# Optimization experiments

Hardware: AMD Instinct MI355X
Metric: run time of the kernel (lower is better)

## Reference

```python
import jax, jax.numpy as jnp
import numpy as np

NEG = jnp.float32(-1e30)  # safe stand-in for -inf in log-space

def setup_inputs() -> dict:
    key = jax.random.key(0)
    k1, k2, k3, k4 = jax.random.split(key, 4)
    N, C, T, S = 64, 64, 4000, 100
    logits = jax.random.normal(k1, (N, C, T), dtype=jnp.float32)
    targets = jax.random.randint(k2, (N, S), 1, C)          # labels, no blank
    target_lengths = jax.random.randint(k3, (N,), 1, S + 1)  # >= 1
    input_lengths = jax.random.randint(k4, (N,), 2000, T + 1)
    return {"logits": logits, "targets": targets,
            "target_lengths": target_lengths, "input_lengths": input_lengths}

def _lse2(a, b):
    m = jnp.maximum(a, b)
    return m + jnp.log(jnp.exp(a - m) + jnp.exp(b - m))

def _lse3(a, b, c):
    m = jnp.maximum(jnp.maximum(a, b), c)
    return m + jnp.log(jnp.exp(a - m) + jnp.exp(b - m) + jnp.exp(c - m))

def reference(logits, targets, target_lengths, input_lengths):
    # logits: (N, C, T); blank = 0; reduction = 'mean' (per-sample / target_len, then mean)
    N, C, T = logits.shape
    S = targets.shape[1]
    L = 2 * S + 1
    lp = jax.nn.log_softmax(logits, axis=1)      # (N, C, T)
    lp = jnp.transpose(lp, (2, 0, 1))            # (T, N, C)

    # extended label sequence: blank, t1, blank, t2, ..., blank  -> (N, L)
    ext = jnp.zeros((N, L), dtype=targets.dtype).at[:, 1::2].set(targets)
    # skip transition s-2 -> s allowed iff ext[s] != blank and ext[s] != ext[s-2]
    prev2 = jnp.pad(ext[:, :-2], ((0, 0), (2, 0)), constant_values=0)
    skip_ok = (ext != 0) & (ext != prev2)        # (N, L)

    # per-time log-probs of extended labels: (T, N, L)
    lp_ext = jnp.take_along_axis(lp, jnp.broadcast_to(ext[None], (T, N, L)), axis=2)

    # alpha init at t=0
    alpha = jnp.full((N, L), NEG, dtype=lp.dtype)
    alpha = alpha.at[:, 0].set(lp_ext[0, :, 0])
    alpha = alpha.at[:, 1].set(lp_ext[0, :, 1])

    neg1 = jnp.full((N, 1), NEG, dtype=lp.dtype)
    neg2 = jnp.full((N, 2), NEG, dtype=lp.dtype)

    def step(a, inp):
        lpt, t = inp                              # lpt: (N, L)
        a1 = a
        a2 = jnp.concatenate([neg1, a[:, :-1]], axis=1)
        a3 = jnp.concatenate([neg2, a[:, :-2]], axis=1)
        a3 = jnp.where(skip_ok, a3, NEG)
        new = _lse3(a1, a2, a3) + lpt
        active = (t < input_lengths)[:, None]     # freeze past input length
        return jnp.where(active, new, a), None

    alpha, _ = jax.lax.scan(step, alpha, (lp_ext[1:], jnp.arange(1, T)))

    i1 = (2 * target_lengths)[:, None]            # last blank
    i2 = jnp.maximum(i1 - 1, 0)                   # last label
    v1 = jnp.take_along_axis(alpha, i1, axis=1)[:, 0]
    v2 = jnp.take_along_axis(alpha, i2, axis=1)[:, 0]
    loss_n = -_lse2(v1, v2)                       # (N,)
    return jnp.mean(loss_n / target_lengths.astype(loss_n.dtype))
```

## Files before the change

kernel.cpp:

```cpp
#include <hip/hip_runtime.h>
#include <cstdint>
#include <cstddef>

#define NEGV (-1e30f)
#define IL2f 1.44269504088896340736f
#define LN2f 0.693147180559945309417f

__device__ __forceinline__ float exp2_hw(float x) { return __builtin_amdgcn_exp2f(x); }
__device__ __forceinline__ float log2_hw(float x) { return __builtin_amdgcn_logf(x); }

constexpr int Nn = 64, Cc = 64, Tt = 4000, Ss = 100;

__device__ __forceinline__ float wave_shr1(float x) {
    return __int_as_float(__builtin_amdgcn_update_dpp(0, __float_as_int(x), 0x138, 0xF, 0xF, true));
}
__device__ __forceinline__ float wave_shl1(float x) {
    return __int_as_float(__builtin_amdgcn_update_dpp(0, __float_as_int(x), 0x130, 0xF, 0xF, true));
}
__device__ __forceinline__ int wave_shr1_i(int x) {
    return __builtin_amdgcn_update_dpp(0, x, 0x138, 0xF, 0xF, true);
}
__device__ __forceinline__ int wave_shl1_i(int x) {
    return __builtin_amdgcn_update_dpp(0, x, 0x130, 0xF, 0xF, true);
}

typedef float f4 __attribute__((ext_vector_type(4)));
typedef float f2 __attribute__((ext_vector_type(2)));
#define LD4(p) (*(const f4*)(p))

__device__ __forceinline__ void gload16(const float* g, float* l) {
    __builtin_amdgcn_global_load_lds(
        (const __attribute__((address_space(1))) void*)g,
        (__attribute__((address_space(3))) void*)l, 16, 0, 0);
}

__global__ __launch_bounds__(256) void ctc_softmax_kernel(
    const float* __restrict__ logits, float* __restrict__ d2, float* __restrict__ P)
{
    const int t4 = (blockIdx.x * 256 + threadIdx.x) * 4;
    const int n = blockIdx.y;
    if (t4 >= Tt) return;
    const float* __restrict__ p = logits + (size_t)n * Cc * Tt + t4;
    f4 m, s;
    {
        f4 v = LD4(p);
        #pragma unroll
        for (int i = 0; i < 4; ++i) { m[i] = v[i] * IL2f; s[i] = 1.f; }
    }
    #pragma unroll 4
    for (int c = 1; c < Cc; ++c) {
        f4 v = LD4(p + (size_t)c * Tt);
        #pragma unroll
        for (int i = 0; i < 4; ++i) {
            float vi = v[i] * IL2f;
            float nm = fmaxf(m[i], vi);
            s[i] = s[i] * exp2_hw(m[i] - nm) + exp2_hw(vi - nm);
            m[i] = nm;
        }
    }
    f4 d;
    #pragma unroll
    for (int i = 0; i < 4; ++i) d[i] = m[i] + log2_hw(s[i]);
    *(f4*)(d2 + (size_t)n * Tt + t4) = d;
    if (P) {
        float* __restrict__ dst = P + (size_t)n * Cc * Tt + t4;
        #pragma unroll 4
        for (int c = 0; c < Cc; ++c) {
            f4 v = LD4(p + (size_t)c * Tt);
            f4 o;
            #pragma unroll
            for (int i = 0; i < 4; ++i) o[i] = exp2_hw(fmaf(v[i], IL2f, -d[i]));
            *(f4*)(dst + (size_t)c * Tt) = o;
        }
    }
}

template<bool PRE>
__global__ __launch_bounds__(64) void ctc_fb_kernel(
    const float* __restrict__ PR, const int* __restrict__ targets,
    const int* __restrict__ tlen, const int* __restrict__ ilen,
    const float* __restrict__ d2, float* __restrict__ wsA, float* __restrict__ wsB)
{
    constexpr int NA = PRE ? 3 : 4;
    constexpr int NLD = NA * 4;
    __shared__ float lds[3][NA][4][64][4];

    const int bid = blockIdx.x;
    const int n = bid >> 1;
    const bool bwd = bid & 1;
    const int lane = threadIdx.x;
    const int tl = tlen[n];
    const int Tn = ilen[n];
    const int L = 2 * tl + 1;
    const int mid = Tn >> 1;
    const int s0 = 4 * lane;

    const int j1 = min(2 * lane, Ss - 1);
    const int j3 = min(2 * lane + 1, Ss - 1);
    const int base = n * Ss;
    const int tg1 = targets[base + j1];
    const int tg3 = targets[base + j3];
    const int tg1m = targets[base + max(2 * lane - 1, 0)];
    const int tg3p = targets[base + min(2 * lane + 2, Ss - 1)];

    const float sk1f = ((s0 + 1 >= 3) && (tg1 != tg1m)) ? 1.f : 0.f;
    const float sk3f = (tg3 != tg1) ? 1.f : 0.f;
    const float sk1b = ((s0 + 3 < L) && (tg3 != tg1)) ? 1.f : 0.f;
    const float sk3b = ((s0 + 5 < L) && (tg3p != tg3)) ? 1.f : 0.f;

    const float* __restrict__ rB = PR + (size_t)(n * Cc) * Tt;
    const float* __restrict__ r1 = PR + (size_t)(n * Cc + tg1) * Tt;
    const float* __restrict__ r3 = PR + (size_t)(n * Cc + tg3) * Tt;
    const float* __restrict__ rD = d2 + (size_t)n * Tt;

    float a0, a1, a2, a3;
    int E = 0;

    if (!bwd) {
        float pB0, p10;
        if constexpr (PRE) { pB0 = rB[0]; p10 = r1[0]; }
        else {
            const float dv = rD[0];
            pB0 = exp2_hw(fmaf(rB[0], IL2f, -dv));
            p10 = exp2_hw(fmaf(r1[0], IL2f, -dv));
        }
        a0 = (lane == 0) ? pB0 : 0.f;
        a1 = (lane == 0) ? p10 : 0.f;
        a2 = 0.f; a3 = 0.f;
    } else {
        const int te = Tn - 1;
        float pBe, p1e, p3e;
        if constexpr (PRE) { pBe = rB[te]; p1e = r1[te]; p3e = r3[te]; }
        else {
            const float dv = rD[te];
            pBe = exp2_hw(fmaf(rB[te], IL2f, -dv));
            p1e = exp2_hw(fmaf(r1[te], IL2f, -dv));
            p3e = exp2_hw(fmaf(r3[te], IL2f, -dv));
        }
        const int sl = 2 * tl;
        a0 = (s0 == sl) ? pBe : 0.f;
        a1 = (s0 + 1 == sl - 1) ? p1e : 0.f;
        a2 = (s0 + 2 == sl) ? pBe : 0.f;
        a3 = (s0 + 3 == sl - 1) ? p3e : 0.f;
    }

    #define ISSUE(gg, sl) {                                                         \
        const int bo_ = (gg) * 16;                                                  \
        _Pragma("unroll")                                                           \
        for (int j = 0; j < 4; ++j) {                                               \
            gload16(rB + bo_ + 4 * j, &lds[sl][0][j][0][0]);                        \
            gload16(r1 + bo_ + 4 * j, &lds[sl][1][j][0][0]);                        \
            gload16(r3 + bo_ + 4 * j, &lds[sl][2][j][0][0]);                        \
            if constexpr (!PRE) gload16(rD + bo_ + 4 * j, &lds[sl][NA - 1][j][0][0]); \
        }                                                                           \
    }
    #define WAITG() asm volatile("s_waitcnt vmcnt(%0)" :: "n"(2 * NLD) : "memory")
    #define LOADREGS(slc)                                                           \
        f4 vB[4], vU[4], vW[4], vD[4];                                              \
        _Pragma("unroll")                                                           \
        for (int j = 0; j < 4; ++j) {                                               \
            vB[j] = LD4(&lds[slc][0][j][lane][0]);                                  \
            vU[j] = LD4(&lds[slc][1][j][lane][0]);                                  \
            vW[j] = LD4(&lds[slc][2][j][lane][0]);                                  \
            if constexpr (!PRE) vD[j] = LD4(&lds[slc][NA - 1][j][lane][0]);         \
        }                                                                           \
        (void)vD;

    #define RENORM_S(nb) {                                                          \
        const float mx = fmaxf(fmaxf(a0, a1), fmaxf(a2, a3));                       \
        const int me = (int)(__float_as_uint(mx) >> 23);                            \
        const float s2 = __int_as_float((unsigned)(254 - me) << 23);                \
        a0 *= s2; a1 *= s2; a2 *= s2; a3 *= s2;                                     \
        E = (mx > 0.f) ? (E + me - 127) : (nb);                                     \
    }

    if (!bwd) {
        const int tB = mid;
        const int gHi = tB >> 4;

        #define BODY_F_G(gg) {                                                      \
            _Pragma("unroll")                                                       \
            for (int w = 0; w < 2; ++w) {                                           \
                const int Eu = wave_shr1_i(E);                                      \
                const int eb = min(max(127 + (Eu - E), 0), 230);                    \
                const float sc = __int_as_float((unsigned)eb << 23);                \
                const float sk1fs = sk1f * sc;                                      \
                _Pragma("unroll")                                                   \
                for (int kk = 0; kk < 8; ++kk) {                                    \
                    const int k = w * 8 + kk;                                       \
                    const int t = (gg) * 16 + k;                                    \
                    if (t >= 1 && t <= tB) {                                        \
                        float pB, p1, p3;                                           \
                        if constexpr (PRE) {                                        \
                            pB = vB[k >> 2][k & 3]; p1 = vU[k >> 2][k & 3];         \
                            p3 = vW[k >> 2][k & 3];                                 \
                        } else {                                                    \
                            const float dv = vD[k >> 2][k & 3];                     \
                            pB = exp2_hw(fmaf(vB[k >> 2][k & 3], IL2f, -dv));       \
                            p1 = exp2_hw(fmaf(vU[k >> 2][k & 3], IL2f, -dv));       \
                            p3 = exp2_hw(fmaf(vW[k >> 2][k & 3], IL2f, -dv));       \
                        }                                                           \
                        const float u3 = wave_shr1(a3);                             \
                        const float n3 = fmaf(a1, sk3f, a3 + a2) * p3;              \
                        const float n2 = (a2 + a1) * pB;                            \
                        const float n1 = fmaf(u3, sk1fs, a1 + a0) * p1;             \
                        const float n0 = fmaf(u3, sc, a0) * pB;                     \
                        a0 = n0; a1 = n1; a2 = n2; a3 = n3;                         \
                    }                                                               \
                }                                                                   \
                RENORM_S(Eu);                                                       \
            }                                                                       \
        }

        #define BODY_F_F() {                                                        \
            f2 Q0 = {a0, a2}, Q1 = {a1, a3};                                        \
            _Pragma("unroll")                                                       \
            for (int w = 0; w < 2; ++w) {                                           \
                const int Eu = wave_shr1_i(E);                                      \
                const int eb = min(max(127 + (Eu - E), 0), 230);                    \
                const float sc = __int_as_float((unsigned)eb << 23);                \
                const f2 Ksk = {sk3f, sk1f * sc};                                   \
                const f2 K1s = {1.0f, sc};                                          \
                _Pragma("unroll")                                                   \
                for (int kk = 0; kk < 8; ++kk) {                                    \
                    const int k = w * 8 + kk;                                       \
                    const float pB = vB[k >> 2][k & 3];                             \
                    const f2 P31 = {vW[k >> 2][k & 3], vU[k >> 2][k & 3]};          \
                    const f2 PBB = {pB, pB};                                        \
                    const float u3 = wave_shr1(Q1.y);                               \
                    const f2 M = {Q1.x, u3};                                        \
                    const f2 Q0s = __builtin_shufflevector(Q0, Q0, 1, 0);           \
                    const f2 S = __builtin_shufflevector(Q1, Q1, 1, 0) + Q0s;       \
                    const f2 F = __builtin_elementwise_fma(M, Ksk, S);              \
                    const f2 G = __builtin_elementwise_fma(M, K1s, Q0s);            \
                    const f2 N31 = F * P31;                                         \
                    const f2 N20 = G * PBB;                                         \
                    Q1 = __builtin_shufflevector(N31, N31, 1, 0);                   \
                    Q0 = __builtin_shufflevector(N20, N20, 1, 0);                   \
                }                                                                   \
                const f2 mxv = __builtin_elementwise_max(Q0, Q1);                   \
                const float mx = fmaxf(mxv.x, mxv.y);                               \
                const int me = (int)(__float_as_uint(mx) >> 23);                    \
                const float s2 = __int_as_float((unsigned)(254 - me) << 23);        \
                const f2 S2 = {s2, s2};                                             \
                Q0 *= S2; Q1 *= S2;                                                 \
                E = (mx > 0.f) ? (E + me - 127) : Eu;                               \
            }                                                                       \
            a0 = Q0.x; a2 = Q0.y; a1 = Q1.x; a3 = Q1.y;                             \
        }

        ISSUE(0, 0);
        ISSUE(min(1, gHi), 1);
        int sli = 2, slc = 0;
        for (int g = 0; g <= gHi; ++g) {
            ISSUE(min(g + 2, gHi), sli);
            sli = (sli == 2) ? 0 : sli + 1;
            WAITG();
            LOADREGS(slc);
            slc = (slc == 2) ? 0 : slc + 1;
            if (PRE && g >= 1 && g * 16 + 15 <= tB) { BODY_F_F(); }
            else                                    { BODY_F_G(g); }
        }
        #undef BODY_F_G
        #undef BODY_F_F
    } else {
        const int tB = Tn - 2, tA = mid + 1;
        const int gHi = tB >> 4, gLo = tA >> 4;

        #define BODY_B_G(gg) {                                                      \
            _Pragma("unroll")                                                       \
            for (int w = 1; w >= 0; --w) {                                          \
                const int Ed = wave_shl1_i(E);                                      \
                const int eb = min(max(127 + (Ed - E), 0), 230);                    \
                const float sc = __int_as_float((unsigned)eb << 23);                \
                const float sk3bs = sk3b * sc;                                      \
                _Pragma("unroll")                                                   \
                for (int kk = 7; kk >= 0; --kk) {                                   \
                    const int k = w * 8 + kk;                                       \
                    const int t = (gg) * 16 + k;                                    \
                    if (t >= tA && t <= tB) {                                       \
                        float pB, p1, p3;                                           \
                        if constexpr (PRE) {                                        \
                            pB = vB[k >> 2][k & 3]; p1 = vU[k >> 2][k & 3];         \
                            p3 = vW[k >> 2][k & 3];                                 \
                        } else {                                                    \
                            const float dv = vD[k >> 2][k & 3];                     \
                            pB = exp2_hw(fmaf(vB[k >> 2][k & 3], IL2f, -dv));       \
                            p1 = exp2_hw(fmaf(vU[k >> 2][k & 3], IL2f, -dv));       \
                            p3 = exp2_hw(fmaf(vW[k >> 2][k & 3], IL2f, -dv));       \
                        }                                                           \
                        const float d0 = wave_shl1(a0);                             \
                        const float d1 = wave_shl1(a1);                             \
                        const float n0 = (a0 + a1) * pB;                            \
                        const float n1 = fmaf(a3, sk1b, a1 + a2) * p1;              \
                        const float n2 = (a2 + a3) * pB;                            \
                        const float n3 = fmaf(d1, sk3bs, fmaf(d0, sc, a3)) * p3;    \
                        a0 = n0; a1 = n1; a2 = n2; a3 = n3;                         \
                    }                                                               \
                }                                                                   \
                RENORM_S(Ed);                                                       \
            }                                                                       \
        }

        #define BODY_B_F() {                                                        \
            f2 Q0 = {a0, a2}, Q1 = {a1, a3};                                        \
            _Pragma("unroll")                                                       \
            for (int w = 1; w >= 0; --w) {                                          \
                const int Ed = wave_shl1_i(E);                                      \
                const int eb = min(max(127 + (Ed - E), 0), 230);                    \
                const float sc = __int_as_float((unsigned)eb << 23);                \
                const f2 K1s = {1.0f, sc};                                          \
                const f2 Ksk = {sk1b, sk3b * sc};                                   \
                _Pragma("unroll")                                                   \
                for (int kk = 7; kk >= 0; --kk) {                                   \
                    const int k = w * 8 + kk;                                       \
                    const float pB = vB[k >> 2][k & 3];                             \
                    const f2 P13 = {vU[k >> 2][k & 3], vW[k >> 2][k & 3]};          \
                    const f2 PBB = {pB, pB};                                        \
                    const float d0 = wave_shl1(Q0.x);                               \
                    const float d1 = wave_shl1(Q1.x);                               \
                    const f2 S = Q0 + Q1;                                           \
                    const f2 A2 = __builtin_elementwise_fma((f2){Q0.y, d0}, K1s, Q1); \
                    const f2 B2 = __builtin_elementwise_fma((f2){Q1.y, d1}, Ksk, A2); \
                    Q1 = B2 * P13;                                                  \
                    Q0 = S * PBB;                                                   \
                }                                                                   \
                const f2 mxv = __builtin_elementwise_max(Q0, Q1);                   \
                const float mx = fmaxf(mxv.x, mxv.y);                               \
                const int me = (int)(__float_as_uint(mx) >> 23);                    \
                const float s2 = __int_as_float((unsigned)(254 - me) << 23);        \
                const f2 S2 = {s2, s2};                                             \
                Q0 *= S2; Q1 *= S2;                                                 \
                E = (mx > 0.f) ? (E + me - 127) : Ed;                               \
            }                                                                       \
            a0 = Q0.x; a2 = Q0.y; a1 = Q1.x; a3 = Q1.y;                             \
        }

        ISSUE(gHi, 0);
        ISSUE(max(gHi - 1, 0), 1);
        int sli = 2, slc = 0;
        for (int g = gHi; g >= gLo; --g) {
            ISSUE(max(g - 2, 0), sli);
            sli = (sli == 2) ? 0 : sli + 1;
            WAITG();
            LOADREGS(slc);
            slc = (slc == 2) ? 0 : slc + 1;
            if (PRE && g * 16 >= tA && g * 16 + 15 <= tB) { BODY_B_F(); }
            else                                          { BODY_B_G(g); }
        }
        #undef BODY_B_G
        #undef BODY_B_F
    }
    #undef ISSUE
    #undef WAITG
    #undef LOADREGS
    #undef RENORM_S

    float* dst = (bwd ? wsB : wsA) + n * 256;
    const float Ef = (float)E;
    f4 o;
    o[0] = (s0     < L && a0 > 0.f) ? log2_hw(a0) + Ef : NEGV;
    o[1] = (s0 + 1 < L && a1 > 0.f) ? log2_hw(a1) + Ef : NEGV;
    o[2] = (s0 + 2 < L && a2 > 0.f) ? log2_hw(a2) + Ef : NEGV;
    o[3] = (s0 + 3 < L && a3 > 0.f) ? log2_hw(a3) + Ef : NEGV;
    *(f4*)(dst + s0) = o;
}

__global__ __launch_bounds__(64) void ctc_combine_kernel(
    const float* __restrict__ wsA, const float* __restrict__ wsB,
    const int* __restrict__ targets, const int* __restrict__ tlen,
    float* __restrict__ out)
{
    const int n = blockIdx.x;
    const int lane = threadIdx.x;
    const int tl = tlen[n];
    const int L = 2 * tl + 1;
    float vals[4];
    float vmax = NEGV;
    #pragma unroll
    for (int k = 0; k < 4; ++k) {
        const int s = lane + (k << 6);
        float v = NEGV;
        if (s < L) {
            const float al = wsA[n * 256 + s];
            const float b0 = wsB[n * 256 + s];
            const float b1 = (s + 1 < L) ? wsB[n * 256 + s + 1] : NEGV;
            const bool skip = (s & 1) && (s + 2 < L) &&
                (targets[n * Ss + (s >> 1) + 1] != targets[n * Ss + (s >> 1)]);
            const float b2 = skip ? wsB[n * 256 + s + 2] : NEGV;
            const float m3 = fmaxf(fmaxf(b0, b1), b2);
            const float B = m3 + log2_hw(exp2_hw(b0 - m3) + exp2_hw(b1 - m3) + exp2_hw(b2 - m3));
            v = al + B;
        }
        vals[k] = v;
        vmax = fmaxf(vmax, v);
    }
    #pragma unroll
    for (int o = 32; o; o >>= 1) vmax = fmaxf(vmax, __shfl_xor(vmax, o));
    float ssum = 0.f;
    #pragma unroll
    for (int k = 0; k < 4; ++k) ssum += exp2_hw(vals[k] - vmax);
    #pragma unroll
    for (int o = 32; o; o >>= 1) ssum += __shfl_xor(ssum, o);
    if (lane == 0) {
        const float total2 = vmax + log2_hw(ssum);
        const float loss = -LN2f * total2;
        atomicAdd(out, loss / ((float)tl * (float)Nn));
    }
}

extern "C" void kernel_launch(void* const* d_in, const int* in_sizes, int n_in,
                              void* d_out, int out_size, void* d_ws, size_t ws_size,
                              hipStream_t stream) {
    const float* logits = (const float*)d_in[0];
    const int* targets  = (const int*)d_in[1];
    const int* tlen     = (const int*)d_in[2];
    const int* ilen     = (const int*)d_in[3];
    float* out = (float*)d_out;

    float* wsA = (float*)d_ws;
    float* wsB = wsA + Nn * 256;
    float* d2  = wsB + Nn * 256;
    float* P   = d2 + (size_t)Nn * Tt;
    const size_t need = ((size_t)Nn * 256 * 2 + (size_t)Nn * Tt
                         + (size_t)Nn * Cc * Tt) * sizeof(float);
    const bool pre = (ws_size >= need);

    hipMemsetAsync(d_out, 0, sizeof(float), stream);
    ctc_softmax_kernel<<<dim3(4, Nn), 256, 0, stream>>>(logits, d2, pre ? P : nullptr);
    if (pre) {
        ctc_fb_kernel<true><<<Nn * 2, 64, 0, stream>>>(P, targets, tlen, ilen, d2, wsA, wsB);
    } else {
        ctc_fb_kernel<false><<<Nn * 2, 64, 0, stream>>>(logits, targets, tlen, ilen, d2, wsA, wsB);
    }
    ctc_combine_kernel<<<Nn, 64, 0, stream>>>(wsA, wsB, targets, tlen, out);
}
```

Baseline: 120.3 us.

## Split probability precompute into parallel kernel and double-buffer 32-step chunks

The softmax kernel is split in two: one kernel computes per-time log-denominators, and a new kernel, launched over an extra grid dimension of channel groups, writes the normalized probabilities. This gives the probability pass more parallelism than the single 256-block launch. The forward-backward kernel's async LDS prefetch changes from a triple-buffered 16-timestep pipeline to a double-buffered 32-timestep one, so it issues fewer waits and loop iterations. In exchange it adds a kernel launch, a re-read of the logits, more registers for the larger LOADREGS arrays, and a shallower prefetch depth.

```diff
diff --git a/kernel.cpp b/kernel.cpp
--- a/kernel.cpp
+++ b/kernel.cpp
@@ -34,8 +34,8 @@
         (__attribute__((address_space(3))) void*)l, 16, 0, 0);
 }
 
-__global__ __launch_bounds__(256) void ctc_softmax_kernel(
-    const float* __restrict__ logits, float* __restrict__ d2, float* __restrict__ P)
+__global__ __launch_bounds__(256) void ctc_denom_kernel(
+    const float* __restrict__ logits, float* __restrict__ d2)
 {
     const int t4 = (blockIdx.x * 256 + threadIdx.x) * 4;
     const int n = blockIdx.y;
@@ -58,20 +58,29 @@
             m[i] = nm;
         }
     }
-    f4 d;
-    #pragma unroll
-    for (int i = 0; i < 4; ++i) d[i] = m[i] + log2_hw(s[i]);
-    *(f4*)(d2 + (size_t)n * Tt + t4) = d;
-    if (P) {
-        float* __restrict__ dst = P + (size_t)n * Cc * Tt + t4;
-        #pragma unroll 4
-        for (int c = 0; c < Cc; ++c) {
-            f4 v = LD4(p + (size_t)c * Tt);
-            f4 o;
-            #pragma unroll
-            for (int i = 0; i < 4; ++i) o[i] = exp2_hw(fmaf(v[i], IL2f, -d[i]));
-            *(f4*)(dst + (size_t)c * Tt) = o;
-        }
+    f4 o;
+    #pragma unroll
+    for (int i = 0; i < 4; ++i) o[i] = m[i] + log2_hw(s[i]);
+    *(f4*)(d2 + (size_t)n * Tt + t4) = o;
+}
+
+__global__ __launch_bounds__(256) void ctc_prob_kernel(
+    const float* __restrict__ logits, const float* __restrict__ d2, float* __restrict__ P)
+{
+    const int t4 = (blockIdx.x * 256 + threadIdx.x) * 4;
+    const int n = blockIdx.y;
+    const int c0 = blockIdx.z * 8;
+    if (t4 >= Tt) return;
+    const f4 d = LD4(d2 + (size_t)n * Tt + t4);
+    const float* __restrict__ src = logits + ((size_t)n * Cc + c0) * Tt + t4;
+    float* __restrict__ dst = P + ((size_t)n * Cc + c0) * Tt + t4;
+    #pragma unroll
+    for (int c = 0; c < 8; ++c) {
+        f4 v = LD4(src + (size_t)c * Tt);
+        f4 o;
+        #pragma unroll
+        for (int i = 0; i < 4; ++i) o[i] = exp2_hw(fmaf(v[i], IL2f, -d[i]));
+        *(f4*)(dst + (size_t)c * Tt) = o;
     }
 }
 
@@ -82,8 +91,8 @@
     const float* __restrict__ d2, float* __restrict__ wsA, float* __restrict__ wsB)
 {
     constexpr int NA = PRE ? 3 : 4;
-    constexpr int NLD = NA * 4;
-    __shared__ float lds[3][NA][4][64][4];
+    constexpr int NLD = NA * 8;
+    __shared__ float lds[2][NA][8][64][4];
 
     const int bid = blockIdx.x;
     const int n = bid >> 1;
@@ -145,20 +154,20 @@
     }
 
     #define ISSUE(gg, sl) {                                                         \
-        const int bo_ = (gg) * 16;                                                  \
+        const int bo_ = (gg) * 32;                                                  \
         _Pragma("unroll")                                                           \
-        for (int j = 0; j < 4; ++j) {                                               \
+        for (int j = 0; j < 8; ++j) {                                               \
             gload16(rB + bo_ + 4 * j, &lds[sl][0][j][0][0]);                        \
             gload16(r1 + bo_ + 4 * j, &lds[sl][1][j][0][0]);                        \
             gload16(r3 + bo_ + 4 * j, &lds[sl][2][j][0][0]);                        \
             if constexpr (!PRE) gload16(rD + bo_ + 4 * j, &lds[sl][NA - 1][j][0][0]); \
         }                                                                           \
     }
-    #define WAITG() asm volatile("s_waitcnt vmcnt(%0)" :: "n"(2 * NLD) : "memory")
+    #define WAITG() asm volatile("s_waitcnt vmcnt(%0)" :: "n"(NLD) : "memory")
     #define LOADREGS(slc)                                                           \
-        f4 vB[4], vU[4], vW[4], vD[4];                                              \
+        f4 vB[8], vU[8], vW[8], vD[8];                                              \
         _Pragma("unroll")                                                           \
-        for (int j = 0; j < 4; ++j) {                                               \
+        for (int j = 0; j < 8; ++j) {                                               \
             vB[j] = LD4(&lds[slc][0][j][lane][0]);                                  \
             vU[j] = LD4(&lds[slc][1][j][lane][0]);                                  \
             vW[j] = LD4(&lds[slc][2][j][lane][0]);                                  \
@@ -176,11 +185,11 @@
 
     if (!bwd) {
         const int tB = mid;
-        const int gHi = tB >> 4;
+        const int gHi = tB >> 5;
 
         #define BODY_F_G(gg) {                                                      \
             _Pragma("unroll")                                                       \
-            for (int w = 0; w < 2; ++w) {                                           \
+            for (int w = 0; w < 4; ++w) {                                           \
                 const int Eu = wave_shr1_i(E);                                      \
                 const int eb = min(max(127 + (Eu - E), 0), 230);                    \
                 const float sc = __int_as_float((unsigned)eb << 23);                \
@@ -188,7 +197,7 @@
                 _Pragma("unroll")                                                   \
                 for (int kk = 0; kk < 8; ++kk) {                                    \
                     const int k = w * 8 + kk;                                       \
-                    const int t = (gg) * 16 + k;                                    \
+                    const int t = (gg) * 32 + k;                                    \
                     if (t >= 1 && t <= tB) {                                        \
                         float pB, p1, p3;                                           \
                         if constexpr (PRE) {                                        \
@@ -215,7 +224,7 @@
         #define BODY_F_F() {                                                        \
             f2 Q0 = {a0, a2}, Q1 = {a1, a3};                                        \
             _Pragma("unroll")                                                       \
-            for (int w = 0; w < 2; ++w) {                                           \
+            for (int w = 0; w < 4; ++w) {                                           \
                 const int Eu = wave_shr1_i(E);                                      \
                 const int eb = min(max(127 + (Eu - E), 0), 230);                    \
                 const float sc = __int_as_float((unsigned)eb << 23);                \
@@ -250,26 +259,24 @@
         }
 
         ISSUE(0, 0);
-        ISSUE(min(1, gHi), 1);
-        int sli = 2, slc = 0;
+        int cur = 0;
         for (int g = 0; g <= gHi; ++g) {
-            ISSUE(min(g + 2, gHi), sli);
-            sli = (sli == 2) ? 0 : sli + 1;
+            ISSUE(min(g + 1, gHi), cur ^ 1);
             WAITG();
-            LOADREGS(slc);
-            slc = (slc == 2) ? 0 : slc + 1;
-            if (PRE && g >= 1 && g * 16 + 15 <= tB) { BODY_F_F(); }
+            LOADREGS(cur);
+            cur ^= 1;
+            if (PRE && g >= 1 && g * 32 + 31 <= tB) { BODY_F_F(); }
             else                                    { BODY_F_G(g); }
         }
         #undef BODY_F_G
         #undef BODY_F_F
     } else {
         const int tB = Tn - 2, tA = mid + 1;
-        const int gHi = tB >> 4, gLo = tA >> 4;
+        const int gHi = tB >> 5, gLo = tA >> 5;
 
         #define BODY_B_G(gg) {                                                      \
             _Pragma("unroll")                                                       \
-            for (int w = 1; w >= 0; --w) {                                          \
+            for (int w = 3; w >= 0; --w) {                                          \
                 const int Ed = wave_shl1_i(E);                                      \
                 const int eb = min(max(127 + (Ed - E), 0), 230);                    \
                 const float sc = __int_as_float((unsigned)eb << 23);                \
@@ -277,7 +284,7 @@
                 _Pragma("unroll")                                                   \
                 for (int kk = 7; kk >= 0; --kk) {                                   \
                     const int k = w * 8 + kk;                                       \
-                    const int t = (gg) * 16 + k;                                    \
+                    const int t = (gg) * 32 + k;                                    \
                     if (t >= tA && t <= tB) {                                       \
                         float pB, p1, p3;                                           \
                         if constexpr (PRE) {                                        \
@@ -305,7 +312,7 @@
         #define BODY_B_F() {                                                        \
             f2 Q0 = {a0, a2}, Q1 = {a1, a3};                                        \
             _Pragma("unroll")                                                       \
-            for (int w = 1; w >= 0; --w) {                                          \
+            for (int w = 3; w >= 0; --w) {                                          \
                 const int Ed = wave_shl1_i(E);                                      \
                 const int eb = min(max(127 + (Ed - E), 0), 230);                    \
                 const float sc = __int_as_float((unsigned)eb << 23);                \
@@ -337,15 +344,13 @@
         }
 
         ISSUE(gHi, 0);
-        ISSUE(max(gHi - 1, 0), 1);
-        int sli = 2, slc = 0;
+        int cur = 0;
         for (int g = gHi; g >= gLo; --g) {
-            ISSUE(max(g - 2, 0), sli);
-            sli = (sli == 2) ? 0 : sli + 1;
+            ISSUE(max(g - 1, 0), cur ^ 1);
             WAITG();
-            LOADREGS(slc);
-            slc = (slc == 2) ? 0 : slc + 1;
-            if (PRE && g * 16 >= tA && g * 16 + 15 <= tB) { BODY_B_F(); }
+            LOADREGS(cur);
+            cur ^= 1;
+            if (PRE && g * 32 >= tA && g * 32 + 31 <= tB) { BODY_B_F(); }
             else                                          { BODY_B_G(g); }
         }
         #undef BODY_B_G
@@ -427,8 +432,9 @@
     const bool pre = (ws_size >= need);
 
     hipMemsetAsync(d_out, 0, sizeof(float), stream);
-    ctc_softmax_kernel<<<dim3(4, Nn), 256, 0, stream>>>(logits, d2, pre ? P : nullptr);
+    ctc_denom_kernel<<<dim3(4, Nn), 256, 0, stream>>>(logits, d2);
     if (pre) {
+        ctc_prob_kernel<<<dim3(4, Nn, 8), 256, 0, stream>>>(logits, d2, P);
         ctc_fb_kernel<true><<<Nn * 2, 64, 0, stream>>>(P, targets, tlen, ilen, d2, wsA, wsB);
     } else {
         ctc_fb_kernel<false><<<Nn * 2, 64, 0, stream>>>(logits, targets, tlen, ilen, d2, wsA, wsB);
```

Measured after the change: 120.2 us. Within noise of the previous version (-0.1%).
